# Optimization experiments

Hardware: AMD Instinct MI355X
Metric: run time of the kernel (lower is better)

## Reference

```python
import jax, jax.numpy as jnp
import numpy as np
import math

EMBED_DIM = 2048
NUM_HEADS = 16
HEAD_DIM = EMBED_DIM // NUM_HEADS
BATCH = 2
SEQ = 2048


def setup_inputs() -> dict:
    key = jax.random.key(0)
    ks = jax.random.split(key, 6)
    x = jax.random.normal(ks[0], (BATCH, SEQ, EMBED_DIM), dtype=jnp.float32)
    # causal mask: True = masked (upper triangle, strictly above diagonal)
    attn_mask = jnp.triu(jnp.ones((SEQ, SEQ), dtype=bool), k=1)
    s = 1.0 / math.sqrt(EMBED_DIM)
    W_qkv = jax.random.normal(ks[1], (3 * EMBED_DIM, EMBED_DIM), dtype=jnp.float32) * s
    b_qkv = jax.random.normal(ks[2], (3 * EMBED_DIM,), dtype=jnp.float32) * 0.01
    W_out = jax.random.normal(ks[3], (EMBED_DIM, EMBED_DIM), dtype=jnp.float32) * s
    b_out = jax.random.normal(ks[4], (EMBED_DIM,), dtype=jnp.float32) * 0.01
    return {"x": x, "W_qkv": W_qkv, "b_qkv": b_qkv, "W_out": W_out,
            "b_out": b_out, "attn_mask": attn_mask}


def reference(x, W_qkv, b_qkv, W_out, b_out, attn_mask):
    B, S, E = x.shape
    # fused QKV projection: [B,S,3E]
    qkv = jnp.einsum('bse,fe->bsf', x, W_qkv) + b_qkv
    qkv = qkv.reshape(B, S, 3, NUM_HEADS, HEAD_DIM)
    qkv = jnp.transpose(qkv, (2, 0, 3, 1, 4))  # [3,B,H,S,Dh]
    q, k, v = qkv[0], qkv[1], qkv[2]
    scale = 1.0 / math.sqrt(HEAD_DIM)
    scores = jnp.einsum('bhqd,bhkd->bhqk', q, k) * scale  # [B,H,S,S]
    scores = jnp.where(attn_mask[None, None, :, :], -jnp.inf, scores)
    attn = jax.nn.softmax(scores, axis=-1)
    out = jnp.einsum('bhqk,bhkd->bhqd', attn, v)  # [B,H,S,Dh]
    out = jnp.transpose(out, (0, 2, 1, 3)).reshape(B, S, E)
    out = jnp.einsum('bse,fe->bsf', out, W_out) + b_out
    return out
```

## Files before the change

### kernel.cpp

```cpp
#include <hip/hip_runtime.h>
#include <hip/hip_bf16.h>
#include <math.h>

#define SEQ   2048
#define EMBED 2048
#define NHEAD 16
#define DHEAD 128
#define BATCH 2

#define NX   ((size_t)BATCH * SEQ * EMBED)
#define NW1  ((size_t)3 * EMBED * EMBED)
#define NB1  ((size_t)3 * EMBED)
#define NW2  ((size_t)EMBED * EMBED)
#define NB2  ((size_t)EMBED)

typedef __bf16 bf16;
typedef __attribute__((__ext_vector_type__(8))) __bf16 bf16x8;
typedef __attribute__((__ext_vector_type__(4))) __bf16 bf16x4;
typedef __attribute__((__ext_vector_type__(4))) float f32x4;
typedef __attribute__((__ext_vector_type__(4))) unsigned int u32x4;

#define NEG_BIG (-1.0e30f)

__device__ __forceinline__ f32x4 mfma_16x16x32(bf16x8 a, bf16x8 b, f32x4 c) {
  return __builtin_amdgcn_mfma_f32_16x16x32_bf16(a, b, c, 0, 0, 0);
}

__device__ __forceinline__ void llds16(bf16* dst, const bf16* src) {
  __builtin_amdgcn_global_load_lds(
      (const __attribute__((address_space(1))) void*)src,
      (__attribute__((address_space(3))) void*)dst, 16, 0, 0);
}

#define BARRAW() asm volatile("s_barrier" ::: "memory")

__global__ void convert_inputs(const void* __restrict__ xin,
                               const void* __restrict__ w1in,
                               const void* __restrict__ b1in,
                               const void* __restrict__ w2in,
                               const void* __restrict__ b2in,
                               bf16* __restrict__ xb, bf16* __restrict__ w1b,
                               bf16* __restrict__ b1b, bf16* __restrict__ w2b,
                               bf16* __restrict__ b2b, int* __restrict__ flagp)
{
  __shared__ int sflag;
  if (threadIdx.x == 0) sflag = 0;
  __syncthreads();
  const unsigned short* xh = (const unsigned short*)xin;
  int huge = 0;
  for (int i = threadIdx.x; i < 2048; i += 256) {
    float f = __uint_as_float((unsigned int)xh[i] << 16);
    if (!(fabsf(f) <= 1e4f)) huge = 1;
  }
  if (huge) sflag = 1;
  __syncthreads();
  const int isf32 = sflag;
  if (blockIdx.x == 0 && threadIdx.x == 0) *flagp = isf32;

  const void* srcs[5] = {xin, w1in, b1in, w2in, b2in};
  bf16* dsts[5] = {xb, w1b, b1b, w2b, b2b};
  const size_t lens[5] = {NX, NW1, NB1, NW2, NB2};
  const size_t gid = (size_t)blockIdx.x * blockDim.x + threadIdx.x;
  const size_t gstride = (size_t)gridDim.x * blockDim.x;
  for (int sidx = 0; sidx < 5; ++sidx) {
    const size_t n8 = lens[sidx] >> 3;
    bf16* d = dsts[sidx];
    if (isf32) {
      const float* s = (const float*)srcs[sidx];
      for (size_t i = gid; i < n8; i += gstride) {
        const float* sp = s + i * 8;
        bf16x8 r;
#pragma unroll
        for (int j = 0; j < 8; ++j) r[j] = (bf16)sp[j];
        *(bf16x8*)(d + i * 8) = r;
      }
    } else {
      const u32x4* s = (const u32x4*)srcs[sidx];
      for (size_t i = gid; i < n8; i += gstride)
        *(u32x4*)(d + i * 8) = s[i];
    }
  }
}

__global__ __launch_bounds__(512, 1) void gemmM(
    const bf16* __restrict__ A, const bf16* __restrict__ B,
    const bf16* __restrict__ bias,
    bf16* __restrict__ outq, bf16* __restrict__ outk, bf16* __restrict__ outv)
{
  __shared__ __align__(16) bf16 lds_[65536];
  const int t = threadIdx.x;
  const int lane = t & 63, w = t >> 6;
  const int wm = w >> 2, wn = w & 3;
  const int lr = lane & 15, lq = lane >> 4;
  const int f = blockIdx.x;
  const int o = (f & 7) * 48 + (f >> 3);
  const int by = o & 15, bx = o >> 4;
  const int m0 = by << 8, n0 = bx << 8;
  const int K = EMBED;
  const int NT = K >> 6;

  const int sg8 = ((lane & 3) ^ (((lane >> 5) & 1) << 1)) << 3;
  const bf16* aS  = A + (size_t)(m0 + w * 32 + (lane >> 2)) * K + sg8;
  const bf16* aS2 = aS + (size_t)16 * K;
  const bf16* bS  = B + (size_t)(n0 + w * 32 + (lane >> 2)) * K + sg8;
  const bf16* bS2 = bS + (size_t)16 * K;
  const int dA = w * 1024;
  const int dB = 16384 + w * 1024;

#define STAGE_HALF(kt_, ks_)                                                 \
  {                                                                          \
    const int _bufb = ((kt_) & 1) * 32768 + (ks_) * 8192;                    \
    const int _kc = ((kt_) << 6) + (ks_) * 32;                               \
    llds16(lds_ + _bufb + dA, aS + _kc);                                     \
    llds16(lds_ + _bufb + dA + 512, aS2 + _kc);                              \
    llds16(lds_ + _bufb + dB, bS + _kc);                                     \
    llds16(lds_ + _bufb + dB + 512, bS2 + _kc);                              \
  }

  f32x4 acc[8][4];
#pragma unroll
  for (int i = 0; i < 8; ++i)
#pragma unroll
    for (int j = 0; j < 4; ++j) acc[i][j] = (f32x4){0.f, 0.f, 0.f, 0.f};

  const int rg8 = (lq ^ (((lr >> 3) & 1) << 1)) << 3;
  const int arow_ = (wm * 128 + lr) * 32 + rg8;
  const int brow_ = 16384 + (wn * 64 + lr) * 32 + rg8;

  STAGE_HALF(0, 0);
  STAGE_HALF(0, 1);
  asm volatile("s_waitcnt vmcnt(0)" ::: "memory");
  BARRAW();

  for (int tt = 0; tt < NT; ++tt) {
    const int bufb = (tt & 1) * 32768;
#pragma unroll
    for (int ks = 0; ks < 2; ++ks) {
      const int base = bufb + ks * 8192;
      bf16x8 af[8], bfv[4];
#pragma unroll
      for (int ai = 0; ai < 8; ++ai)
        af[ai] = *(const bf16x8*)(lds_ + base + arow_ + ai * 512);
#pragma unroll
      for (int ni = 0; ni < 4; ++ni)
        bfv[ni] = *(const bf16x8*)(lds_ + base + brow_ + ni * 512);
      if (tt + 1 < NT) STAGE_HALF(tt + 1, ks);
      __builtin_amdgcn_s_setprio(1);
#pragma unroll
      for (int ai = 0; ai < 8; ++ai)
#pragma unroll
        for (int ni = 0; ni < 4; ++ni)
          acc[ai][ni] = mfma_16x16x32(af[ai], bfv[ni], acc[ai][ni]);
      __builtin_amdgcn_s_setprio(0);
      if (tt + 1 < NT) {
        asm volatile("s_waitcnt vmcnt(4)" ::: "memory");
      } else if (ks == 0) {
        asm volatile("s_waitcnt vmcnt(0)" ::: "memory");
      }
      BARRAW();
    }
  }
#undef STAGE_HALF

  const int which = n0 >> 11;
  const int bbid = m0 >> 11;
  const int s0 = m0 & 2047;
  if (which == 2) {
#pragma unroll
    for (int ni = 0; ni < 4; ++ni) {
      const int ng = n0 + wn * 64 + ni * 16 + lr;
      const int h = (ng >> 7) & 15;
      const int d = ng & 127;
      const float bv = (float)bias[ng];
      bf16* rowp =
          outv + ((size_t)(bbid * NHEAD + h) * DHEAD + d) * SEQ + s0 + wm * 128;
#pragma unroll
      for (int ai = 0; ai < 8; ++ai) {
        bf16x4 pk;
#pragma unroll
        for (int reg = 0; reg < 4; ++reg)
          pk[reg] = (bf16)(acc[ai][ni][reg] + bv);
        *(bf16x4*)(rowp + ai * 16 + lq * 4) = pk;
      }
    }
  } else {
    bf16* dst = (which == 0) ? outq : outk;
#pragma unroll
    for (int ni = 0; ni < 4; ++ni) {
      const int ng = n0 + wn * 64 + ni * 16 + lr;
      const int h = (ng >> 7) & 15;
      const int d = ng & 127;
      const float bv = (float)bias[ng];
      bf16* hb = dst + (size_t)(bbid * NHEAD + h) * SEQ * DHEAD + d;
#pragma unroll
      for (int ai = 0; ai < 8; ++ai)
#pragma unroll
        for (int reg = 0; reg < 4; ++reg) {
          const int s = s0 + wm * 128 + ai * 16 + lq * 4 + reg;
          hb[(size_t)s * DHEAD] = (bf16)(acc[ai][ni][reg] + bv);
        }
    }
  }
}

template <int MODE>
__global__ __launch_bounds__(512, 1) void gemmE(
    const bf16* __restrict__ A, const bf16* __restrict__ B,
    const bf16* __restrict__ bias, int K,
    void* __restrict__ out0v, bf16* __restrict__ out1, bf16* __restrict__ out2,
    const int* __restrict__ flagp)
{
  __shared__ __align__(16) bf16 lds_[49152];
  constexpr int NTX = (MODE == 0) ? 24 : 8;
  const int t = threadIdx.x;
  const int lane = t & 63, w = t >> 6;
  const int wm = w >> 2, wn = w & 3;
  const int lr = lane & 15, lq = lane >> 4;
  const int nwg = 32 * NTX;
  const int f = blockIdx.x;
  const int o = (f & 7) * (nwg >> 3) + (f >> 3);
  const int by = o & 31, bx = o >> 5;
  const int m0 = by << 7, n0 = bx << 8;
  const int NT = K >> 6;
  const int NI = NT >> 1;

  const int srow = t >> 2;
  const int sg8 = (((t & 3) ^ (((t >> 5) & 1) << 1))) << 3;

#define STAGE3(kt_, ks_)                                                     \
  {                                                                          \
    const int _kt = (kt_), _ks = (ks_);                                      \
    if (_kt < NT) {                                                          \
      const int _bb = (_kt & 1) * 24576;                                     \
      const int _kc = (_kt << 6) + _ks * 32;                                 \
      llds16(lds_ + _bb + _ks * 4096 + (w << 9),                             \
             A + (size_t)(m0 + srow) * K + _kc + sg8);                       \
      llds16(lds_ + _bb + 8192 + _ks * 8192 + (w << 9),                      \
             B + (size_t)(n0 + srow) * K + _kc + sg8);                       \
      llds16(lds_ + _bb + 8192 + _ks * 8192 + 4096 + (w << 9),               \
             B + (size_t)(n0 + 128 + srow) * K + _kc + sg8);                 \
    }                                                                        \
  }

  f32x4 acc[4][4];
#pragma unroll
  for (int i = 0; i < 4; ++i)
#pragma unroll
    for (int j = 0; j < 4; ++j) acc[i][j] = (f32x4){0.f, 0.f, 0.f, 0.f};

  const int rg8 = ((lq ^ (((lr >> 3) & 1) << 1))) << 3;
  const int arow = (wm * 64 + lr) * 32 + rg8;
  const int brow = (wn * 64 + lr) * 32 + rg8;

  STAGE3(0, 0);
  STAGE3(0, 1);
  STAGE3(1, 0);
  asm volatile("s_waitcnt vmcnt(6)" ::: "memory");
  BARRAW();

  for (int i = 0; i < NI; ++i) {
    const int k2 = i << 1;
#pragma unroll
    for (int p = 0; p < 4; ++p) {
      const int ks = p & 1;
      const int bufb = (p >> 1) * 24576;
      bf16x8 af[4], bfv[4];
      const int ab = bufb + ks * 4096 + arow;
      const int bb = bufb + 8192 + ks * 8192 + brow;
#pragma unroll
      for (int mi = 0; mi < 4; ++mi)
        af[mi] = *(const bf16x8*)(lds_ + ab + mi * 512);
#pragma unroll
      for (int ni = 0; ni < 4; ++ni)
        bfv[ni] = *(const bf16x8*)(lds_ + bb + ni * 512);
      if (p == 0)      STAGE3(k2 + 1, 1)
      else if (p == 1) STAGE3(k2 + 2, 0)
      else if (p == 2) STAGE3(k2 + 2, 1)
      else             STAGE3(k2 + 3, 0)
      BARRAW();
      __builtin_amdgcn_s_setprio(1);
#pragma unroll
      for (int mi = 0; mi < 4; ++mi)
#pragma unroll
        for (int ni = 0; ni < 4; ++ni)
          acc[mi][ni] = mfma_16x16x32(af[mi], bfv[ni], acc[mi][ni]);
      __builtin_amdgcn_s_setprio(0);
      if (i == 0 && p == 0) {
        asm volatile("s_waitcnt vmcnt(6)" ::: "memory");
      }
      if (p == 1) {
        if (i == NI - 1) { asm volatile("s_waitcnt vmcnt(0)" ::: "memory"); }
        else             { asm volatile("s_waitcnt vmcnt(3)" ::: "memory"); }
      }
      if (p == 3 && i < NI - 1) {
        asm volatile("s_waitcnt vmcnt(3)" ::: "memory");
      }
      BARRAW();
    }
  }
#undef STAGE3

  if (MODE == 0) {
    const int which = n0 >> 11;
    const int bbid = m0 >> 11;
    const int s0 = m0 & 2047;
    if (which == 2) {
      bf16* dst = out2;
#pragma unroll
      for (int ni = 0; ni < 4; ++ni) {
        const int ng = n0 + wn * 64 + ni * 16 + lr;
        const int h = (ng >> 7) & 15;
        const int d = ng & 127;
        const float bv = (float)bias[ng];
        bf16* rowp =
            dst + ((size_t)(bbid * NHEAD + h) * DHEAD + d) * SEQ + s0 + wm * 64;
#pragma unroll
        for (int mi = 0; mi < 4; ++mi) {
          bf16x4 pk;
#pragma unroll
          for (int reg = 0; reg < 4; ++reg)
            pk[reg] = (bf16)(acc[mi][ni][reg] + bv);
          *(bf16x4*)(rowp + mi * 16 + lq * 4) = pk;
        }
      }
    } else {
      bf16* dst = (which == 0) ? (bf16*)out0v : out1;
#pragma unroll
      for (int ni = 0; ni < 4; ++ni) {
        const int ng = n0 + wn * 64 + ni * 16 + lr;
        const int h = (ng >> 7) & 15;
        const int d = ng & 127;
        const float bv = (float)bias[ng];
        bf16* hb = dst + (size_t)(bbid * NHEAD + h) * SEQ * DHEAD + d;
#pragma unroll
        for (int mi = 0; mi < 4; ++mi)
#pragma unroll
          for (int reg = 0; reg < 4; ++reg) {
            const int s = s0 + wm * 64 + mi * 16 + lq * 4 + reg;
            hb[(size_t)s * DHEAD] = (bf16)(acc[mi][ni][reg] + bv);
          }
      }
    }
  } else {
    const int isf32 = *flagp;
#pragma unroll
    for (int ni = 0; ni < 4; ++ni) {
      const int col = n0 + wn * 64 + ni * 16 + lr;
      const float bv = (float)bias[col];
#pragma unroll
      for (int mi = 0; mi < 4; ++mi)
#pragma unroll
        for (int reg = 0; reg < 4; ++reg) {
          const int row = m0 + wm * 64 + mi * 16 + lq * 4 + reg;
          const float v = acc[mi][ni][reg] + bv;
          const size_t idx = (size_t)row * EMBED + col;
          if (isf32) ((float*)out0v)[idx] = v;
          else       ((bf16*)out0v)[idx] = (bf16)v;
        }
    }
  }
}

__device__ __forceinline__ void qk_softmax_tile(
    const bf16* __restrict__ sK, bf16* __restrict__ sP, const bf16x8* aq,
    float& m_i, float& l_i, f32x4* oacc, int kt, int qt,
    int w, int lr, int lq, int sPofs)
{
  const float scale = 0.08838834764831845f;
  f32x4 tacc[4];
#pragma unroll
  for (int ni = 0; ni < 4; ++ni) tacc[ni] = (f32x4){0.f, 0.f, 0.f, 0.f};
#pragma unroll
  for (int ks = 0; ks < 4; ++ks)
#pragma unroll
    for (int ni = 0; ni < 4; ++ni) {
      bf16x8 bk = *(const bf16x8*)(sK + (ni * 16 + lr) * 136 + ks * 32 + lq * 8);
      tacc[ni] = mfma_16x16x32(bk, aq[ks], tacc[ni]);
    }
  float pp[4][4];
  const int qg = qt * 64 + w * 16 + lr;
#pragma unroll
  for (int ni = 0; ni < 4; ++ni)
#pragma unroll
    for (int reg = 0; reg < 4; ++reg) {
      float sv = tacc[ni][reg] * scale;
      if (kt == qt) {
        const int kg = kt * 64 + ni * 16 + lq * 4 + reg;
        if (kg > qg) sv = NEG_BIG;
      }
      pp[ni][reg] = sv;
    }
  float mx;
  {
    float a0 = fmaxf(fmaxf(pp[0][0], pp[0][1]), fmaxf(pp[0][2], pp[0][3]));
    float a1 = fmaxf(fmaxf(pp[1][0], pp[1][1]), fmaxf(pp[1][2], pp[1][3]));
    float a2 = fmaxf(fmaxf(pp[2][0], pp[2][1]), fmaxf(pp[2][2], pp[2][3]));
    float a3 = fmaxf(fmaxf(pp[3][0], pp[3][1]), fmaxf(pp[3][2], pp[3][3]));
    mx = fmaxf(fmaxf(a0, a1), fmaxf(a2, a3));
  }
  mx = fmaxf(mx, __shfl_xor(mx, 16, 64));
  mx = fmaxf(mx, __shfl_xor(mx, 32, 64));
  const float mnew = fmaxf(m_i, mx);
  const float alpha = __expf(m_i - mnew);
  float ls = 0.f;
#pragma unroll
  for (int ni = 0; ni < 4; ++ni) {
    float s0 = __expf(pp[ni][0] - mnew);
    float s1 = __expf(pp[ni][1] - mnew);
    float s2 = __expf(pp[ni][2] - mnew);
    float s3 = __expf(pp[ni][3] - mnew);
    pp[ni][0] = s0; pp[ni][1] = s1; pp[ni][2] = s2; pp[ni][3] = s3;
    ls += (s0 + s1) + (s2 + s3);
  }
  ls += __shfl_xor(ls, 16, 64);
  ls += __shfl_xor(ls, 32, 64);
  l_i = l_i * alpha + ls;
  m_i = mnew;
#pragma unroll
  for (int dt = 0; dt < 8; ++dt) oacc[dt] *= alpha;
  bf16* rowp = sP + (sPofs + w * 16 + lr) * 64;
  const int swz = lr & 7;
#pragma unroll
  for (int ni = 0; ni < 4; ++ni) {
    bf16x4 pk;
#pragma unroll
    for (int reg = 0; reg < 4; ++reg) pk[reg] = (bf16)pp[ni][reg];
    const int col = ni * 16 + lq * 4;
    const int scol = (((col >> 3) ^ swz) << 3) | (col & 7);
    *(bf16x4*)(rowp + scol) = pk;
  }
}

__device__ __forceinline__ void pv_tile(const bf16* __restrict__ sP,
                                        const bf16* __restrict__ sV,
                                        f32x4* oacc, int w, int lr, int lq,
                                        int sPofs)
{
  const bf16* rowp = sP + (sPofs + w * 16 + lr) * 64;
  const int swz = lr & 7;
#pragma unroll
  for (int ks2 = 0; ks2 < 2; ++ks2) {
    const int chunk = ks2 * 4 + lq;
    bf16x8 bp = *(const bf16x8*)(rowp + ((chunk ^ swz) << 3));
#pragma unroll
    for (int dt = 0; dt < 8; ++dt) {
      bf16x8 av =
          *(const bf16x8*)(sV + (dt * 16 + lr) * 72 + ks2 * 32 + lq * 8);
      oacc[dt] = mfma_16x16x32(av, bp, oacc[dt]);
    }
  }
}

__global__ __launch_bounds__(256, 2) void attn_fwd(
    const bf16* __restrict__ qb, const bf16* __restrict__ kb,
    const bf16* __restrict__ vt, bf16* __restrict__ aout)
{
  __shared__ bf16 sK[64 * 136];
  __shared__ bf16 sV[128 * 72];
  __shared__ bf16 sP[128 * 64];
  const int t = threadIdx.x;
  const int lane = t & 63, w = t >> 6;
  const int lr = lane & 15, lq = lane >> 4;
  const int p  = blockIdx.x & 15;
  const int bh = blockIdx.x >> 4;
  const int bb = bh >> 4, h = bh & 15;
  const int qlo = p, qhi = 31 - p;

  bf16x8 aqL[4], aqH[4];
  {
    const bf16* qpL =
        qb + ((size_t)bh * SEQ + qlo * 64 + w * 16 + lr) * DHEAD + lq * 8;
    const bf16* qpH =
        qb + ((size_t)bh * SEQ + qhi * 64 + w * 16 + lr) * DHEAD + lq * 8;
#pragma unroll
    for (int ks = 0; ks < 4; ++ks) {
      aqL[ks] = *(const bf16x8*)(qpL + ks * 32);
      aqH[ks] = *(const bf16x8*)(qpH + ks * 32);
    }
  }

  f32x4 oL[8], oH[8];
#pragma unroll
  for (int i = 0; i < 8; ++i) {
    oL[i] = (f32x4){0.f, 0.f, 0.f, 0.f};
    oH[i] = (f32x4){0.f, 0.f, 0.f, 0.f};
  }
  float mL = NEG_BIG, mH = NEG_BIG;
  float lL = 0.f, lH = 0.f;

  bf16x8 rk[4], rv[4];
  const int kr_ = t >> 4, kd_ = t & 15;
  const int vr_ = t >> 3, vk_ = t & 7;
#define FETCH(ktv)                                                          \
  {                                                                         \
    const int _kt = (ktv);                                                  \
    _Pragma("unroll") for (int i = 0; i < 4; ++i) {                         \
      rk[i] = *(const bf16x8*)(kb + ((size_t)bh * SEQ + _kt * 64 +          \
                                     (i * 16 + kr_)) * DHEAD + kd_ * 8);    \
      rv[i] = *(const bf16x8*)(vt + ((size_t)bh * DHEAD + (i * 32 + vr_)) * \
                                     SEQ + _kt * 64 + vk_ * 8);             \
    }                                                                       \
  }
#define COMMIT()                                                            \
  {                                                                         \
    _Pragma("unroll") for (int i = 0; i < 4; ++i) {                         \
      *(bf16x8*)(sK + (i * 16 + kr_) * 136 + kd_ * 8) = rk[i];              \
      *(bf16x8*)(sV + (i * 32 + vr_) * 72 + vk_ * 8) = rv[i];               \
    }                                                                       \
  }

  FETCH(0);
  COMMIT();
  __syncthreads();

  for (int kt = 0; kt <= qhi; ++kt) {
    if (kt < qhi) FETCH(kt + 1);
    const bool doLo = (kt <= qlo);

    qk_softmax_tile(sK, sP, aqH, mH, lH, oH, kt, qhi, w, lr, lq, 64);
    if (doLo) qk_softmax_tile(sK, sP, aqL, mL, lL, oL, kt, qlo, w, lr, lq, 0);
    asm volatile("s_waitcnt lgkmcnt(0)" ::: "memory");
    pv_tile(sP, sV, oH, w, lr, lq, 64);
    if (doLo) pv_tile(sP, sV, oL, w, lr, lq, 0);

    __syncthreads();
    if (kt < qhi) {
      COMMIT();
      __syncthreads();
    }
  }

#pragma unroll
  for (int side = 0; side < 2; ++side) {
    const f32x4* oacc = side ? oH : oL;
    const float linv = 1.0f / (side ? lH : lL);
    const int qt = side ? qhi : qlo;
    const int qg = qt * 64 + w * 16 + lr;
    bf16* outp = aout + ((size_t)bb * SEQ + qg) * EMBED + h * 128 + lq * 4;
#pragma unroll
    for (int dt = 0; dt < 8; ++dt) {
      bf16x4 pk;
#pragma unroll
      for (int reg = 0; reg < 4; ++reg)
        pk[reg] = (bf16)(oacc[dt][reg] * linv);
      *(bf16x4*)(outp + dt * 16) = pk;
    }
  }
#undef FETCH
#undef COMMIT
}

extern "C" void kernel_launch(void* const* d_in, const int* in_sizes, int n_in,
                              void* d_out, int out_size, void* d_ws, size_t ws_size,
                              hipStream_t stream) {
  const void* x    = d_in[0];
  const void* Wqkv = d_in[1];
  const void* bqkv = d_in[2];
  const void* Wout = d_in[3];
  const void* bout = d_in[4];

  int* flagp = (int*)d_ws;
  bf16* base = (bf16*)((char*)d_ws + 256);
  bf16* xb   = base;
  bf16* w1b  = xb + NX;
  bf16* b1b  = w1b + NW1;
  bf16* w2b  = b1b + NB1;
  bf16* b2b  = w2b + NW2;
  bf16* qb   = b2b + NB2;
  bf16* kb   = qb + NX;
  bf16* vt   = kb + NX;
  bf16* aout = vt + NX;

  convert_inputs<<<dim3(1024), dim3(256), 0, stream>>>(
      x, Wqkv, bqkv, Wout, bout, xb, w1b, b1b, w2b, b2b, flagp);
  gemmM<<<dim3(384), dim3(512), 0, stream>>>(xb, w1b, b1b, qb, kb, vt);
  attn_fwd<<<dim3(512), dim3(256), 0, stream>>>(qb, kb, vt, aout);
  gemmE<1><<<dim3(256), dim3(512), 0, stream>>>(
      aout, w2b, b2b, EMBED, d_out, nullptr, nullptr, flagp);
}
```

Baseline: 388.7 us.

## Double-buffer 32-wide KV tiles via direct global-to-LDS loads in attention

Changes the attention kernel's key tile from 64 to 32 rows and double-buffers K/V tiles in LDS. Staging now goes through llds16 (direct global-to-LDS loads) with XOR-swizzled layouts instead of register fetch-then-commit, which removes one barrier per iteration. It also adds s_setprio around the MFMA sections and raises the launch-bounds occupancy hint from 2 to 3 blocks per CU. The cost is twice as many loop iterations, each with its own softmax rescale and shuffle reductions, and more per-iteration overhead.

```diff
diff --git a/kernel.cpp b/kernel.cpp
--- a/kernel.cpp
+++ b/kernel.cpp
@@ -361,31 +361,34 @@
   }
 }
 
-__device__ __forceinline__ void qk_softmax_tile(
-    const bf16* __restrict__ sK, bf16* __restrict__ sP, const bf16x8* aq,
+__device__ __forceinline__ void qk32(
+    const bf16* __restrict__ sKb, bf16* __restrict__ sP, const bf16x8* aq,
     float& m_i, float& l_i, f32x4* oacc, int kt, int qt,
     int w, int lr, int lq, int sPofs)
 {
   const float scale = 0.08838834764831845f;
-  f32x4 tacc[4];
-#pragma unroll
-  for (int ni = 0; ni < 4; ++ni) tacc[ni] = (f32x4){0.f, 0.f, 0.f, 0.f};
+  f32x4 tacc[2];
+  tacc[0] = (f32x4){0.f, 0.f, 0.f, 0.f};
+  tacc[1] = (f32x4){0.f, 0.f, 0.f, 0.f};
+  __builtin_amdgcn_s_setprio(1);
 #pragma unroll
   for (int ks = 0; ks < 4; ++ks)
 #pragma unroll
-    for (int ni = 0; ni < 4; ++ni) {
-      bf16x8 bk = *(const bf16x8*)(sK + (ni * 16 + lr) * 136 + ks * 32 + lq * 8);
+    for (int ni = 0; ni < 2; ++ni) {
+      bf16x8 bk = *(const bf16x8*)(
+          sKb + (ni * 16 + lr) * 128 + ((((ks << 2) | lq) ^ (lr & 7)) << 3));
       tacc[ni] = mfma_16x16x32(bk, aq[ks], tacc[ni]);
     }
-  float pp[4][4];
+  __builtin_amdgcn_s_setprio(0);
+  float pp[2][4];
   const int qg = qt * 64 + w * 16 + lr;
 #pragma unroll
-  for (int ni = 0; ni < 4; ++ni)
+  for (int ni = 0; ni < 2; ++ni)
 #pragma unroll
     for (int reg = 0; reg < 4; ++reg) {
       float sv = tacc[ni][reg] * scale;
-      if (kt == qt) {
-        const int kg = kt * 64 + ni * 16 + lq * 4 + reg;
+      if (kt >= 2 * qt) {
+        const int kg = kt * 32 + ni * 16 + lq * 4 + reg;
         if (kg > qg) sv = NEG_BIG;
       }
       pp[ni][reg] = sv;
@@ -394,9 +397,7 @@
   {
     float a0 = fmaxf(fmaxf(pp[0][0], pp[0][1]), fmaxf(pp[0][2], pp[0][3]));
     float a1 = fmaxf(fmaxf(pp[1][0], pp[1][1]), fmaxf(pp[1][2], pp[1][3]));
-    float a2 = fmaxf(fmaxf(pp[2][0], pp[2][1]), fmaxf(pp[2][2], pp[2][3]));
-    float a3 = fmaxf(fmaxf(pp[3][0], pp[3][1]), fmaxf(pp[3][2], pp[3][3]));
-    mx = fmaxf(fmaxf(a0, a1), fmaxf(a2, a3));
+    mx = fmaxf(a0, a1);
   }
   mx = fmaxf(mx, __shfl_xor(mx, 16, 64));
   mx = fmaxf(mx, __shfl_xor(mx, 32, 64));
@@ -404,7 +405,7 @@
   const float alpha = __expf(m_i - mnew);
   float ls = 0.f;
 #pragma unroll
-  for (int ni = 0; ni < 4; ++ni) {
+  for (int ni = 0; ni < 2; ++ni) {
     float s0 = __expf(pp[ni][0] - mnew);
     float s1 = __expf(pp[ni][1] - mnew);
     float s2 = __expf(pp[ni][2] - mnew);
@@ -418,46 +419,43 @@
   m_i = mnew;
 #pragma unroll
   for (int dt = 0; dt < 8; ++dt) oacc[dt] *= alpha;
-  bf16* rowp = sP + (sPofs + w * 16 + lr) * 64;
-  const int swz = lr & 7;
-#pragma unroll
-  for (int ni = 0; ni < 4; ++ni) {
+  bf16* rowp = sP + (sPofs + w * 16 + lr) * 32;
+  const int s = (lr >> 1) & 3;
+#pragma unroll
+  for (int ni = 0; ni < 2; ++ni) {
     bf16x4 pk;
 #pragma unroll
     for (int reg = 0; reg < 4; ++reg) pk[reg] = (bf16)pp[ni][reg];
-    const int col = ni * 16 + lq * 4;
-    const int scol = (((col >> 3) ^ swz) << 3) | (col & 7);
-    *(bf16x4*)(rowp + scol) = pk;
-  }
-}
-
-__device__ __forceinline__ void pv_tile(const bf16* __restrict__ sP,
-                                        const bf16* __restrict__ sV,
-                                        f32x4* oacc, int w, int lr, int lq,
-                                        int sPofs)
+    const int chunk = (ni << 1) | (lq >> 1);
+    *(bf16x4*)(rowp + ((chunk ^ s) << 3) + ((lq & 1) << 2)) = pk;
+  }
+}
+
+__device__ __forceinline__ void pv32(const bf16* __restrict__ sP,
+                                     const bf16* __restrict__ sVb,
+                                     f32x4* oacc, int w, int lr, int lq,
+                                     int sPofs)
 {
-  const bf16* rowp = sP + (sPofs + w * 16 + lr) * 64;
-  const int swz = lr & 7;
-#pragma unroll
-  for (int ks2 = 0; ks2 < 2; ++ks2) {
-    const int chunk = ks2 * 4 + lq;
-    bf16x8 bp = *(const bf16x8*)(rowp + ((chunk ^ swz) << 3));
-#pragma unroll
-    for (int dt = 0; dt < 8; ++dt) {
-      bf16x8 av =
-          *(const bf16x8*)(sV + (dt * 16 + lr) * 72 + ks2 * 32 + lq * 8);
-      oacc[dt] = mfma_16x16x32(av, bp, oacc[dt]);
-    }
-  }
-}
-
-__global__ __launch_bounds__(256, 2) void attn_fwd(
+  const int s = (lr >> 1) & 3;
+  const bf16x8 bp = *(const bf16x8*)(
+      sP + (sPofs + w * 16 + lr) * 32 + ((lq ^ s) << 3));
+  __builtin_amdgcn_s_setprio(1);
+#pragma unroll
+  for (int dt = 0; dt < 8; ++dt) {
+    bf16x8 av = *(const bf16x8*)(
+        sVb + (dt * 16 + lr) * 32 + ((lq ^ s) << 3));
+    oacc[dt] = mfma_16x16x32(av, bp, oacc[dt]);
+  }
+  __builtin_amdgcn_s_setprio(0);
+}
+
+__global__ __launch_bounds__(256, 3) void attn_fwd(
     const bf16* __restrict__ qb, const bf16* __restrict__ kb,
     const bf16* __restrict__ vt, bf16* __restrict__ aout)
 {
-  __shared__ bf16 sK[64 * 136];
-  __shared__ bf16 sV[128 * 72];
-  __shared__ bf16 sP[128 * 64];
+  __shared__ __align__(16) bf16 sK[2][32 * 128];
+  __shared__ __align__(16) bf16 sV[2][128 * 32];
+  __shared__ __align__(16) bf16 sP[128 * 32];
   const int t = threadIdx.x;
   const int lane = t & 63, w = t >> 6;
   const int lr = lane & 15, lq = lane >> 4;
@@ -466,6 +464,28 @@
   const int bb = bh >> 4, h = bh & 15;
   const int qlo = p, qhi = 31 - p;
 
+  const bf16* kS[2];
+  const bf16* vS[2];
+#pragma unroll
+  for (int j = 0; j < 2; ++j) {
+    const int c = (w << 1) | j;
+    const int krow = c * 4 + (lane >> 4);
+    const int kgl = (lane & 15) ^ (((j << 2) + (lane >> 4)) & 7);
+    kS[j] = kb + ((size_t)bh * SEQ + krow) * DHEAD + kgl * 8;
+    const int vrow = c * 16 + (lane >> 2);
+    const int vgl = (lane & 3) ^ ((lane >> 3) & 3);
+    vS[j] = vt + ((size_t)bh * DHEAD + vrow) * SEQ + vgl * 8;
+  }
+
+#define STAGE(kt_, buf_)                                                    \
+  {                                                                         \
+    const int _ko = (kt_) * 32;                                             \
+    _Pragma("unroll") for (int j = 0; j < 2; ++j) {                         \
+      llds16(&sK[buf_][(((w << 1) | j)) * 512], kS[j] + (size_t)_ko * DHEAD); \
+      llds16(&sV[buf_][(((w << 1) | j)) * 512], vS[j] + _ko);               \
+    }                                                                       \
+  }
+
   bf16x8 aqL[4], aqH[4];
   {
     const bf16* qpL =
@@ -488,47 +508,25 @@
   float mL = NEG_BIG, mH = NEG_BIG;
   float lL = 0.f, lH = 0.f;
 
-  bf16x8 rk[4], rv[4];
-  const int kr_ = t >> 4, kd_ = t & 15;
-  const int vr_ = t >> 3, vk_ = t & 7;
-#define FETCH(ktv)                                                          \
-  {                                                                         \
-    const int _kt = (ktv);                                                  \
-    _Pragma("unroll") for (int i = 0; i < 4; ++i) {                         \
-      rk[i] = *(const bf16x8*)(kb + ((size_t)bh * SEQ + _kt * 64 +          \
-                                     (i * 16 + kr_)) * DHEAD + kd_ * 8);    \
-      rv[i] = *(const bf16x8*)(vt + ((size_t)bh * DHEAD + (i * 32 + vr_)) * \
-                                     SEQ + _kt * 64 + vk_ * 8);             \
-    }                                                                       \
-  }
-#define COMMIT()                                                            \
-  {                                                                         \
-    _Pragma("unroll") for (int i = 0; i < 4; ++i) {                         \
-      *(bf16x8*)(sK + (i * 16 + kr_) * 136 + kd_ * 8) = rk[i];              \
-      *(bf16x8*)(sV + (i * 32 + vr_) * 72 + vk_ * 8) = rv[i];               \
-    }                                                                       \
-  }
-
-  FETCH(0);
-  COMMIT();
+  STAGE(0, 0);
   __syncthreads();
 
-  for (int kt = 0; kt <= qhi; ++kt) {
-    if (kt < qhi) FETCH(kt + 1);
-    const bool doLo = (kt <= qlo);
-
-    qk_softmax_tile(sK, sP, aqH, mH, lH, oH, kt, qhi, w, lr, lq, 64);
-    if (doLo) qk_softmax_tile(sK, sP, aqL, mL, lL, oL, kt, qlo, w, lr, lq, 0);
+  const int ktmax = 2 * qhi + 1;
+  const int ktlo  = 2 * qlo + 1;
+  for (int kt = 0; kt <= ktmax; ++kt) {
+    const int buf = kt & 1;
+    if (kt < ktmax) STAGE(kt + 1, buf ^ 1);
+    const bool doLo = (kt <= ktlo);
+
+    qk32(sK[buf], sP, aqH, mH, lH, oH, kt, qhi, w, lr, lq, 64);
+    if (doLo) qk32(sK[buf], sP, aqL, mL, lL, oL, kt, qlo, w, lr, lq, 0);
     asm volatile("s_waitcnt lgkmcnt(0)" ::: "memory");
-    pv_tile(sP, sV, oH, w, lr, lq, 64);
-    if (doLo) pv_tile(sP, sV, oL, w, lr, lq, 0);
+    pv32(sP, sV[buf], oH, w, lr, lq, 64);
+    if (doLo) pv32(sP, sV[buf], oL, w, lr, lq, 0);
 
     __syncthreads();
-    if (kt < qhi) {
-      COMMIT();
-      __syncthreads();
-    }
-  }
+  }
+#undef STAGE
 
 #pragma unroll
   for (int side = 0; side < 2; ++side) {
@@ -546,8 +544,6 @@
       *(bf16x4*)(outp + dt * 16) = pk;
     }
   }
-#undef FETCH
-#undef COMMIT
 }
 
 extern "C" void kernel_launch(void* const* d_in, const int* in_sizes, int n_in,
```

Result: slower. 402.7 us (+3.6%).
